# Performance work log

Hardware: AMD Instinct MI355X
Metric: run time of the kernel (lower is better)

Reference implementation:

```python
import jax, jax.numpy as jnp
import numpy as np

N, E, B = 50000, 1600000, 64
VOCAB, EMB = 1000, 16
HID, OUT_FEAT = 192, 128   # hidden_sf*model_dim, out_sf*output_channels
MODEL_DIM, DEMO, OUT_DIM = 64, 5, 2
EPS = 1e-7  # GENConv eps


def setup_inputs() -> dict:
    key = jax.random.key(0)
    ks = jax.random.split(key, 18)
    f32 = jnp.float32

    def rn(k, shape, scale):
        return jax.random.normal(k, shape, dtype=f32) * scale

    node_idx = jax.random.randint(ks[0], (N,), 0, VOCAB)
    edge_index = jax.random.randint(ks[1], (2, E), 0, N)
    batch = jnp.sort(jax.random.randint(ks[2], (N,), 0, B))
    demographics = rn(ks[3], (B, DEMO), 1.0)

    emb = rn(ks[4], (VOCAB, EMB), 1.0)
    dims = [(EMB, HID), (HID, HID), (HID, HID), (HID, OUT_FEAT)]
    params = {}
    for i, (din, dout) in enumerate(dims):
        params[f"W{i}"] = rn(ks[5 + 2 * i], (din, dout), 1.0 / np.sqrt(din))
        params[f"b{i}"] = jnp.zeros((dout,), f32)
    params["Wc1"] = rn(ks[13], (OUT_FEAT + DEMO, MODEL_DIM), 1.0 / np.sqrt(OUT_FEAT + DEMO))
    params["bc1"] = jnp.zeros((MODEL_DIM,), f32)
    params["Wc2"] = rn(ks[14], (MODEL_DIM, OUT_DIM), 1.0 / np.sqrt(MODEL_DIM))
    params["bc2"] = jnp.zeros((OUT_DIM,), f32)

    return {"node_idx": node_idx, "edge_index": edge_index, "batch": batch,
            "demographics": demographics, "emb": emb, **params}


def _gen_conv(x, src, dst, W, b):
    # GENConv (num_layers=1, aggr='add', edge_attr=None):
    #   out_i = Linear( sum_{j->i} (relu(x_j) + eps) + x_i )
    m = jax.nn.relu(x) + EPS                                   # [N, D]
    agg = jax.ops.segment_sum(m[src], dst, num_segments=x.shape[0])
    return (agg + x) @ W + b


def reference(node_idx, edge_index, batch, demographics, emb,
              W0, b0, W1, b1, W2, b2, W3, b3, Wc1, bc1, Wc2, bc2):
    x = emb[node_idx]                                          # [N, 16]
    src, dst = edge_index[0], edge_index[1]
    for W, b in ((W0, b0), (W1, b1), (W2, b2), (W3, b3)):
        x = _gen_conv(x, src, dst, W, b)                       # [N, D_l]
    # global_mean_pool
    cnt = jax.ops.segment_sum(jnp.ones((x.shape[0],), x.dtype), batch, num_segments=B)
    g = jax.ops.segment_sum(x, batch, num_segments=B) / jnp.maximum(cnt, 1.0)[:, None]
    feats = jnp.concatenate([g, demographics], axis=1)         # [B, 133]
    h = jax.nn.relu(feats @ Wc1 + bc1)                         # dropout = identity (eval)
    return h @ Wc2 + bc2                                       # [B, out_dim]
```

## Files before the change

kernel.cpp:

```cpp
#include <hip/hip_runtime.h>
#include <stdint.h>

#define EPS 1e-7f

constexpr int N_NODES = 50000;
constexpr int N_EDGES = 1600000;
constexpr int BATCH = 64;
constexpr int EMB = 16;
constexpr int HID = 192;
constexpr int OUTF = 128;
constexpr int DEMO = 5;
constexpr int MODEL_DIM = 64;
constexpr int OUT_DIM = 2;

constexpr int NPART = 8;
constexpr int PART_NODES = (N_NODES + NPART - 1) / NPART;

constexpr int NBKT = 16;
constexpr int BKT_DIV = (N_NODES + NBKT - 1) / NBKT;
constexpr int NB2 = N_NODES * NBKT;

constexpr int SCAN2_CHUNK = 1024;
constexpr int NCHUNK2 = (NB2 + SCAN2_CHUNK - 1) / SCAN2_CHUNK;

typedef unsigned short bf16_t;
typedef unsigned short u16;
typedef short s8v __attribute__((ext_vector_type(8)));
typedef float f4v __attribute__((ext_vector_type(4)));

static __device__ __forceinline__ float bf2f(bf16_t u) {
  return __uint_as_float(((uint32_t)u) << 16);
}
static __device__ __forceinline__ bf16_t f2bf(float f) {
  uint32_t b = __float_as_uint(f);
  return (bf16_t)((b + 0x7FFFu + ((b >> 16) & 1u)) >> 16);
}

__global__ void emb_gather(const int* __restrict__ idx, const float* __restrict__ emb,
                           bf16_t* __restrict__ x) {
  int t = blockIdx.x * blockDim.x + threadIdx.x;
  if (t >= N_NODES * EMB) return;
  int node = t / EMB, f = t % EMB;
  x[t] = f2bf(emb[idx[node] * EMB + f]);
}

__global__ void hist2_kernel(const int* __restrict__ src, const int* __restrict__ dst,
                             int* __restrict__ hist2) {
  int part = blockIdx.x & (NPART - 1);
  int blk = blockIdx.x >> 3;
  int nthread = (gridDim.x >> 3) * blockDim.x;
  int lo = part * PART_NODES, hi = lo + PART_NODES;
  for (int e = blk * blockDim.x + threadIdx.x; e < N_EDGES; e += nthread) {
    int d = dst[e];
    if (d >= lo && d < hi) atomicAdd(&hist2[d * NBKT + src[e] / BKT_DIV], 1);
  }
}

__global__ void chunk_sum2_kernel(const int* __restrict__ hist2, int* __restrict__ chunk_sum) {
  int t = threadIdx.x;
  int base = blockIdx.x * SCAN2_CHUNK + t * 4;
  int v = 0;
#pragma unroll
  for (int j = 0; j < 4; ++j) {
    int i = base + j;
    if (i < NB2) v += hist2[i];
  }
#pragma unroll
  for (int off = 32; off > 0; off >>= 1) v += __shfl_down(v, off);
  __shared__ int s[4];
  if ((t & 63) == 0) s[t >> 6] = v;
  __syncthreads();
  if (t == 0) chunk_sum[blockIdx.x] = s[0] + s[1] + s[2] + s[3];
}

__global__ void scan_chunks2_kernel(const int* __restrict__ chunk_sum,
                                    int* __restrict__ chunk_off) {
  __shared__ int s[1024];
  int t = threadIdx.x;
  int v = (t < NCHUNK2) ? chunk_sum[t] : 0;
  s[t] = v;
  __syncthreads();
  for (int off = 1; off < 1024; off <<= 1) {
    int u = (t >= off) ? s[t - off] : 0;
    __syncthreads();
    s[t] += u;
    __syncthreads();
  }
  if (t < NCHUNK2) chunk_off[t] = s[t] - v;
}

__global__ void chunk_scan_write2_kernel(const int* __restrict__ hist2,
                                         const int* __restrict__ chunk_off,
                                         int* __restrict__ cursor2,
                                         int* __restrict__ row_start) {
  __shared__ int s[256];
  int t = threadIdx.x;
  int base = blockIdx.x * SCAN2_CHUNK + t * 4;
  int local[4];
  int tsum = 0;
#pragma unroll
  for (int j = 0; j < 4; ++j) {
    int i = base + j;
    local[j] = (i < NB2) ? hist2[i] : 0;
    tsum += local[j];
  }
  s[t] = tsum;
  __syncthreads();
  for (int off = 1; off < 256; off <<= 1) {
    int u = (t >= off) ? s[t - off] : 0;
    __syncthreads();
    s[t] += u;
    __syncthreads();
  }
  int run = chunk_off[blockIdx.x] + s[t] - tsum;
#pragma unroll
  for (int j = 0; j < 4; ++j) {
    int i = base + j;
    if (i < NB2) {
      cursor2[i] = run;
      if ((i & (NBKT - 1)) == 0) row_start[i / NBKT] = run;
      if (i == NB2 - 1) row_start[N_NODES] = run + local[j];
      run += local[j];
    }
  }
}

__global__ void scatter_kernel(const int* __restrict__ src, const int* __restrict__ dst,
                               int* __restrict__ cursor2, u16* __restrict__ csr_src) {
  int part = blockIdx.x & (NPART - 1);
  int blk = blockIdx.x >> 3;
  int nthread = (gridDim.x >> 3) * blockDim.x;
  int lo = part * PART_NODES, hi = lo + PART_NODES;
  for (int e = blk * blockDim.x + threadIdx.x; e < N_EDGES; e += nthread) {
    int d = dst[e];
    if (d >= lo && d < hi) {
      int s = src[e];
      int pos = atomicAdd(&cursor2[d * NBKT + s / BKT_DIV], 1);
      csr_src[pos] = (u16)s;
    }
  }
}

template <int TPN, int NPB>
__global__ void agg2_kernel(const uint32_t* __restrict__ x, const int* __restrict__ row_start,
                            const u16* __restrict__ csr_src, uint32_t* __restrict__ out) {
  int f = threadIdx.x % TPN;
  int node = blockIdx.x * NPB + threadIdx.x / TPN;
  if (node >= N_NODES) return;
  int s0 = row_start[node], s1 = row_start[node + 1];
  float deps = (float)(s1 - s0) * EPS;
  uint32_t xv = x[(size_t)node * TPN + f];
  float a0 = __uint_as_float(xv << 16) + deps;
  float a1 = __uint_as_float(xv & 0xFFFF0000u) + deps;
  int e = s0;
  for (; e + 8 <= s1; e += 8) {
    int idx[8];
#pragma unroll
    for (int j = 0; j < 8; ++j) idx[j] = csr_src[e + j];
    uint32_t v[8];
#pragma unroll
    for (int j = 0; j < 8; ++j) v[j] = x[(size_t)idx[j] * TPN + f];
#pragma unroll
    for (int j = 0; j < 8; ++j) {
      a0 += fmaxf(__uint_as_float(v[j] << 16), 0.f);
      a1 += fmaxf(__uint_as_float(v[j] & 0xFFFF0000u), 0.f);
    }
  }
  for (; e < s1; ++e) {
    uint32_t v = x[(size_t)csr_src[e] * TPN + f];
    a0 += fmaxf(__uint_as_float(v << 16), 0.f);
    a1 += fmaxf(__uint_as_float(v & 0xFFFF0000u), 0.f);
  }
  out[(size_t)node * TPN + f] = (uint32_t)f2bf(a0) | ((uint32_t)f2bf(a1) << 16);
}

__global__ void wprep_kernel(const float* __restrict__ W, int K, int NOUT,
                             bf16_t* __restrict__ Wt) {
  int t = blockIdx.x * blockDim.x + threadIdx.x;
  if (t >= K * NOUT) return;
  int k = t / NOUT, n = t % NOUT;
  Wt[(size_t)n * K + k] = f2bf(W[t]);
}

constexpr int FU_TPN = 24;
constexpr int FU_NPB = 16;
constexpr int FU_LDR = 200;
template <int NOUT, bool OUT_BF16>
__global__ void fused_agg_gemm(const uint4* __restrict__ x, const int* __restrict__ row_start,
                               const u16* __restrict__ csr_src,
                               const bf16_t* __restrict__ Wt, const float* __restrict__ bias,
                               void* __restrict__ outp) {
  constexpr int K = 192;
  constexpr int ROW = 24;
  __shared__ bf16_t tile[FU_NPB * FU_LDR];

  {
    int f = threadIdx.x % FU_TPN;
    int ln = threadIdx.x / FU_TPN;
    int node = blockIdx.x * FU_NPB + ln;
    int s0 = row_start[node], s1 = row_start[node + 1];
    float deps = (float)(s1 - s0) * EPS;
    uint4 xv = x[(size_t)node * ROW + f];
    float a[8];
    {
      uint32_t pk[4] = {xv.x, xv.y, xv.z, xv.w};
#pragma unroll
      for (int q = 0; q < 4; ++q) {
        a[2 * q]     = __uint_as_float(pk[q] << 16) + deps;
        a[2 * q + 1] = __uint_as_float(pk[q] & 0xFFFF0000u) + deps;
      }
    }
    int e = s0;
    for (; e + 4 <= s1; e += 4) {
      int idx[4];
#pragma unroll
      for (int j = 0; j < 4; ++j) idx[j] = csr_src[e + j];
      uint4 v[4];
#pragma unroll
      for (int j = 0; j < 4; ++j) v[j] = x[(size_t)idx[j] * ROW + f];
#pragma unroll
      for (int j = 0; j < 4; ++j) {
        uint32_t pk[4] = {v[j].x, v[j].y, v[j].z, v[j].w};
#pragma unroll
        for (int q = 0; q < 4; ++q) {
          a[2 * q]     += fmaxf(__uint_as_float(pk[q] << 16), 0.f);
          a[2 * q + 1] += fmaxf(__uint_as_float(pk[q] & 0xFFFF0000u), 0.f);
        }
      }
    }
    for (; e < s1; ++e) {
      uint4 v = x[(size_t)csr_src[e] * ROW + f];
      uint32_t pk[4] = {v.x, v.y, v.z, v.w};
#pragma unroll
      for (int q = 0; q < 4; ++q) {
        a[2 * q]     += fmaxf(__uint_as_float(pk[q] << 16), 0.f);
        a[2 * q + 1] += fmaxf(__uint_as_float(pk[q] & 0xFFFF0000u), 0.f);
      }
    }
    uint4 o;
    o.x = (uint32_t)f2bf(a[0]) | ((uint32_t)f2bf(a[1]) << 16);
    o.y = (uint32_t)f2bf(a[2]) | ((uint32_t)f2bf(a[3]) << 16);
    o.z = (uint32_t)f2bf(a[4]) | ((uint32_t)f2bf(a[5]) << 16);
    o.w = (uint32_t)f2bf(a[6]) | ((uint32_t)f2bf(a[7]) << 16);
    *reinterpret_cast<uint4*>(&tile[ln * FU_LDR + f * 8]) = o;
  }
  __syncthreads();

  {
    constexpr int KT = K / 32;
    constexpr int NT = NOUT / 16;
    int wave = threadIdx.x >> 6;
    int lane = threadIdx.x & 63;
    int rlo = lane & 15;
    int kbase = (lane >> 4) * 8;

    s8v af[KT];
#pragma unroll
    for (int kt = 0; kt < KT; ++kt)
      af[kt] = *reinterpret_cast<const s8v*>(&tile[rlo * FU_LDR + kbase + kt * 32]);

    int r0 = (lane >> 4) * 4;
    for (int nt = wave; nt < NT; nt += 6) {
      const bf16_t* wp = Wt + ((size_t)(nt * 16 + rlo)) * K + kbase;
      f4v c = {0.f, 0.f, 0.f, 0.f};
#pragma unroll
      for (int kt = 0; kt < KT; ++kt) {
        s8v b = *(const s8v*)(wp + kt * 32);
        c = __builtin_amdgcn_mfma_f32_16x16x32_bf16(af[kt], b, c, 0, 0, 0);
      }
      int col = nt * 16 + rlo;
      float bv = bias[col];
#pragma unroll
      for (int r = 0; r < 4; ++r) {
        float v = c[r] + bv;
        size_t o = (size_t)(blockIdx.x * FU_NPB + r0 + r) * NOUT + col;
        if constexpr (OUT_BF16) ((bf16_t*)outp)[o] = f2bf(v);
        else                    ((float*)outp)[o] = v;
      }
    }
  }
}

template <int DIN, int DOUT, bool OUT_BF16>
__global__ void gemm_kernel(const bf16_t* __restrict__ in, const float* __restrict__ W,
                            const float* __restrict__ bias, void* __restrict__ outp) {
  constexpr int ROWS = 16;
  __shared__ bf16_t tile[ROWS * DIN];
  int c = threadIdx.x;
  int base = blockIdx.x * ROWS;

  {
    const uint4* gsrc = reinterpret_cast<const uint4*>(in + (size_t)base * DIN);
    uint4* ldst = reinterpret_cast<uint4*>(tile);
    constexpr int NV = ROWS * DIN * 2 / 16;
    for (int i = threadIdx.x; i < NV; i += blockDim.x) ldst[i] = gsrc[i];
  }
  __syncthreads();

  float acc[ROWS];
  float bc = bias[c];
#pragma unroll
  for (int r = 0; r < ROWS; ++r) acc[r] = bc;

  for (int k0 = 0; k0 < DIN; k0 += 8) {
    float w[8];
#pragma unroll
    for (int j = 0; j < 8; ++j) w[j] = W[(size_t)(k0 + j) * DOUT + c];
#pragma unroll
    for (int r = 0; r < ROWS; ++r) {
      uint4 packed = *reinterpret_cast<const uint4*>(&tile[r * DIN + k0]);
      uint32_t pk[4] = {packed.x, packed.y, packed.z, packed.w};
#pragma unroll
      for (int q = 0; q < 4; ++q) {
        float lo = __uint_as_float(pk[q] << 16);
        float hi = __uint_as_float(pk[q] & 0xFFFF0000u);
        acc[r] = fmaf(lo, w[2 * q], acc[r]);
        acc[r] = fmaf(hi, w[2 * q + 1], acc[r]);
      }
    }
  }

#pragma unroll
  for (int r = 0; r < ROWS; ++r) {
    size_t o = (size_t)(base + r) * DOUT + c;
    if constexpr (OUT_BF16) ((bf16_t*)outp)[o] = f2bf(acc[r]);
    else                    ((float*)outp)[o] = acc[r];
  }
}

constexpr int POOL_CHUNK = 100;
__global__ void pool_kernel(const float* __restrict__ x, const int* __restrict__ batch,
                            float* __restrict__ gsum, int* __restrict__ gcnt) {
  int f = threadIdx.x;
  int start = blockIdx.x * POOL_CHUNK;
  if (start >= N_NODES) return;
  int end = min(start + POOL_CHUNK, N_NODES);
  int cur = batch[start];
  float acc = 0.f;
  int cnt = 0;
  for (int i = start; i < end; ++i) {
    int b = batch[i];
    if (b != cur) {
      atomicAdd(&gsum[cur * OUTF + f], acc);
      if (f == 0) atomicAdd(&gcnt[cur], cnt);
      acc = 0.f; cnt = 0; cur = b;
    }
    acc += x[(size_t)i * OUTF + f];
    cnt++;
  }
  atomicAdd(&gsum[cur * OUTF + f], acc);
  if (f == 0) atomicAdd(&gcnt[cur], cnt);
}

__global__ void mlp_kernel(const float* __restrict__ gsum, const int* __restrict__ gcnt,
                           const float* __restrict__ demo,
                           const float* __restrict__ Wc1, const float* __restrict__ bc1,
                           const float* __restrict__ Wc2, const float* __restrict__ bc2,
                           float* __restrict__ out) {
  int b = blockIdx.x;
  int c = threadIdx.x;
  __shared__ float feats[OUTF + DEMO];
  float inv = 1.f / fmaxf((float)gcnt[b], 1.f);
  for (int k = c; k < OUTF; k += MODEL_DIM) feats[k] = gsum[b * OUTF + k] * inv;
  if (c < DEMO) feats[OUTF + c] = demo[b * DEMO + c];
  __syncthreads();
  float s = bc1[c];
#pragma unroll
  for (int k = 0; k < OUTF + DEMO; ++k) s = fmaf(feats[k], Wc1[k * MODEL_DIM + c], s);
  float h = fmaxf(s, 0.f);
  float o0 = h * Wc2[c * OUT_DIM + 0];
  float o1 = h * Wc2[c * OUT_DIM + 1];
#pragma unroll
  for (int off = 32; off > 0; off >>= 1) {
    o0 += __shfl_down(o0, off);
    o1 += __shfl_down(o1, off);
  }
  if (c == 0) {
    out[b * OUT_DIM + 0] = o0 + bc2[0];
    out[b * OUT_DIM + 1] = o1 + bc2[1];
  }
}

extern "C" void kernel_launch(void* const* d_in, const int* in_sizes, int n_in,
                              void* d_out, int out_size, void* d_ws, size_t ws_size,
                              hipStream_t stream) {
  const int*   node_idx = (const int*)d_in[0];
  const int*   edge_index = (const int*)d_in[1];
  const int*   batch = (const int*)d_in[2];
  const float* demo = (const float*)d_in[3];
  const float* emb  = (const float*)d_in[4];
  const float* W0 = (const float*)d_in[5];  const float* b0 = (const float*)d_in[6];
  const float* W1 = (const float*)d_in[7];  const float* b1 = (const float*)d_in[8];
  const float* W2 = (const float*)d_in[9];  const float* b2 = (const float*)d_in[10];
  const float* W3 = (const float*)d_in[11]; const float* b3 = (const float*)d_in[12];
  const float* Wc1 = (const float*)d_in[13]; const float* bc1 = (const float*)d_in[14];
  const float* Wc2 = (const float*)d_in[15]; const float* bc2 = (const float*)d_in[16];
  const int* src = edge_index;
  const int* dst = edge_index + N_EDGES;
  float* out = (float*)d_out;

  char* ws = (char*)d_ws;
  size_t off = 0;
  auto alloc = [&](size_t bytes) {
    void* p = ws + off;
    off += (bytes + 255) & ~size_t(255);
    return p;
  };
  bf16_t* xbf     = (bf16_t*)alloc((size_t)N_NODES * HID * 2);
  bf16_t* xbf2    = (bf16_t*)alloc((size_t)N_NODES * HID * 2);
  bf16_t* xbf0    = (bf16_t*)alloc((size_t)N_NODES * EMB * 2);
  bf16_t* agg0    = (bf16_t*)alloc((size_t)N_NODES * EMB * 2);
  float*  x3      = (float*)alloc((size_t)N_NODES * OUTF * 4);
  u16*   csr_src  = (u16*)alloc((size_t)N_EDGES * 2);
  int*   hist2    = (int*)alloc((size_t)NB2 * 4);
  int*   cursor2  = (int*)alloc((size_t)NB2 * 4);
  int*   row_start= (int*)alloc((size_t)(N_NODES + 1) * 4);
  int*   chunk_sum= (int*)alloc((size_t)NCHUNK2 * 4);
  int*   chunk_off= (int*)alloc((size_t)NCHUNK2 * 4);
  float* gsum     = (float*)alloc((size_t)BATCH * OUTF * 4);
  int*   gcnt     = (int*)alloc((size_t)BATCH * 4);
  bf16_t* Wt1     = (bf16_t*)alloc((size_t)HID * HID * 2);
  bf16_t* Wt2     = (bf16_t*)alloc((size_t)HID * HID * 2);
  bf16_t* Wt3     = (bf16_t*)alloc((size_t)OUTF * HID * 2);

  hipMemsetAsync(hist2, 0, (size_t)NB2 * 4, stream);
  hipMemsetAsync(gsum, 0, (size_t)BATCH * OUTF * 4, stream);
  hipMemsetAsync(gcnt, 0, (size_t)BATCH * 4, stream);

  wprep_kernel<<<(HID * HID + 255) / 256, 256, 0, stream>>>(W1, HID, HID, Wt1);
  wprep_kernel<<<(HID * HID + 255) / 256, 256, 0, stream>>>(W2, HID, HID, Wt2);
  wprep_kernel<<<(HID * OUTF + 255) / 256, 256, 0, stream>>>(W3, HID, OUTF, Wt3);

  hist2_kernel<<<NPART * 256, 256, 0, stream>>>(src, dst, hist2);
  chunk_sum2_kernel<<<NCHUNK2, 256, 0, stream>>>(hist2, chunk_sum);
  scan_chunks2_kernel<<<1, 1024, 0, stream>>>(chunk_sum, chunk_off);
  chunk_scan_write2_kernel<<<NCHUNK2, 256, 0, stream>>>(hist2, chunk_off, cursor2, row_start);
  scatter_kernel<<<NPART * 256, 256, 0, stream>>>(src, dst, cursor2, csr_src);

  constexpr int FU_GRID = N_NODES / FU_NPB;

  emb_gather<<<(N_NODES * EMB + 255) / 256, 256, 0, stream>>>(node_idx, emb, xbf0);
  agg2_kernel<8, 32><<<(N_NODES + 31) / 32, 256, 0, stream>>>(
      (const uint32_t*)xbf0, row_start, csr_src, (uint32_t*)agg0);
  gemm_kernel<16, 192, true><<<N_NODES / 16, 192, 0, stream>>>(agg0, W0, b0, xbf);
  fused_agg_gemm<192, true><<<FU_GRID, FU_TPN * FU_NPB, 0, stream>>>(
      (const uint4*)xbf, row_start, csr_src, Wt1, b1, xbf2);
  fused_agg_gemm<192, true><<<FU_GRID, FU_TPN * FU_NPB, 0, stream>>>(
      (const uint4*)xbf2, row_start, csr_src, Wt2, b2, xbf);
  fused_agg_gemm<128, false><<<FU_GRID, FU_TPN * FU_NPB, 0, stream>>>(
      (const uint4*)xbf, row_start, csr_src, Wt3, b3, x3);

  pool_kernel<<<(N_NODES + POOL_CHUNK - 1) / POOL_CHUNK, OUTF, 0, stream>>>(x3, batch, gsum, gcnt);
  mlp_kernel<<<BATCH, MODEL_DIM, 0, stream>>>(gsum, gcnt, demo, Wc1, bc1, Wc2, bc2, out);
}
```

Baseline: 487.5 us.

## Sort nodes by in-degree so fused agg-GEMM blocks get balanced work

Builds a degree-binned permutation of nodes (histogram, scan, scatter) and has each fused aggregation+GEMM block process nodes of similar degree, writing outputs to the permuted rows. This targets load imbalance and divergence within blocks, where lanes handling high-degree nodes stall others. It adds three small kernels plus an indirection and scattered output rows, which may lose write locality. With random uniform edges the degrees are near-Poisson around 32, so the imbalance being removed is small.

```diff
diff --git a/kernel.cpp b/kernel.cpp
--- a/kernel.cpp
+++ b/kernel.cpp
@@ -22,6 +22,8 @@
 
 constexpr int SCAN2_CHUNK = 1024;
 constexpr int NCHUNK2 = (NB2 + SCAN2_CHUNK - 1) / SCAN2_CHUNK;
+
+constexpr int NDBIN = 1024;
 
 typedef unsigned short bf16_t;
 typedef unsigned short u16;
@@ -138,6 +140,39 @@
       int pos = atomicAdd(&cursor2[d * NBKT + s / BKT_DIV], 1);
       csr_src[pos] = (u16)s;
     }
+  }
+}
+
+__global__ void dbin_hist_kernel(const int* __restrict__ row_start, int* __restrict__ dhist) {
+  int i = blockIdx.x * blockDim.x + threadIdx.x;
+  if (i < N_NODES) {
+    int deg = row_start[i + 1] - row_start[i];
+    atomicAdd(&dhist[min(deg, NDBIN - 1)], 1);
+  }
+}
+
+__global__ void dbin_scan_kernel(const int* __restrict__ dhist, int* __restrict__ dcur) {
+  __shared__ int s[NDBIN];
+  int t = threadIdx.x;
+  int v = dhist[t];
+  s[t] = v;
+  __syncthreads();
+  for (int off = 1; off < NDBIN; off <<= 1) {
+    int u = (t >= off) ? s[t - off] : 0;
+    __syncthreads();
+    s[t] += u;
+    __syncthreads();
+  }
+  dcur[t] = s[t] - v;
+}
+
+__global__ void dbin_scatter_kernel(const int* __restrict__ row_start, int* __restrict__ dcur,
+                                    int* __restrict__ perm) {
+  int i = blockIdx.x * blockDim.x + threadIdx.x;
+  if (i < N_NODES) {
+    int deg = row_start[i + 1] - row_start[i];
+    int pos = atomicAdd(&dcur[min(deg, NDBIN - 1)], 1);
+    perm[pos] = i;
   }
 }
 
@@ -187,17 +222,19 @@
 constexpr int FU_LDR = 200;
 template <int NOUT, bool OUT_BF16>
 __global__ void fused_agg_gemm(const uint4* __restrict__ x, const int* __restrict__ row_start,
-                               const u16* __restrict__ csr_src,
+                               const u16* __restrict__ csr_src, const int* __restrict__ perm,
                                const bf16_t* __restrict__ Wt, const float* __restrict__ bias,
                                void* __restrict__ outp) {
   constexpr int K = 192;
   constexpr int ROW = 24;
   __shared__ bf16_t tile[FU_NPB * FU_LDR];
+  __shared__ int nodemap[FU_NPB];
 
   {
     int f = threadIdx.x % FU_TPN;
     int ln = threadIdx.x / FU_TPN;
-    int node = blockIdx.x * FU_NPB + ln;
+    int node = perm[blockIdx.x * FU_NPB + ln];
+    if (f == 0) nodemap[ln] = node;
     int s0 = row_start[node], s1 = row_start[node + 1];
     float deps = (float)(s1 - s0) * EPS;
     uint4 xv = x[(size_t)node * ROW + f];
@@ -260,6 +297,10 @@
       af[kt] = *reinterpret_cast<const s8v*>(&tile[rlo * FU_LDR + kbase + kt * 32]);
 
     int r0 = (lane >> 4) * 4;
+    int orow[4];
+#pragma unroll
+    for (int r = 0; r < 4; ++r) orow[r] = nodemap[r0 + r];
+
     for (int nt = wave; nt < NT; nt += 6) {
       const bf16_t* wp = Wt + ((size_t)(nt * 16 + rlo)) * K + kbase;
       f4v c = {0.f, 0.f, 0.f, 0.f};
@@ -273,7 +314,7 @@
 #pragma unroll
       for (int r = 0; r < 4; ++r) {
         float v = c[r] + bv;
-        size_t o = (size_t)(blockIdx.x * FU_NPB + r0 + r) * NOUT + col;
+        size_t o = (size_t)orow[r] * NOUT + col;
         if constexpr (OUT_BF16) ((bf16_t*)outp)[o] = f2bf(v);
         else                    ((float*)outp)[o] = v;
       }
@@ -417,6 +458,9 @@
   int*   row_start= (int*)alloc((size_t)(N_NODES + 1) * 4);
   int*   chunk_sum= (int*)alloc((size_t)NCHUNK2 * 4);
   int*   chunk_off= (int*)alloc((size_t)NCHUNK2 * 4);
+  int*   dhist    = (int*)alloc((size_t)NDBIN * 4);
+  int*   dcur     = (int*)alloc((size_t)NDBIN * 4);
+  int*   perm     = (int*)alloc((size_t)N_NODES * 4);
   float* gsum     = (float*)alloc((size_t)BATCH * OUTF * 4);
   int*   gcnt     = (int*)alloc((size_t)BATCH * 4);
   bf16_t* Wt1     = (bf16_t*)alloc((size_t)HID * HID * 2);
@@ -424,6 +468,7 @@
   bf16_t* Wt3     = (bf16_t*)alloc((size_t)OUTF * HID * 2);
 
   hipMemsetAsync(hist2, 0, (size_t)NB2 * 4, stream);
+  hipMemsetAsync(dhist, 0, (size_t)NDBIN * 4, stream);
   hipMemsetAsync(gsum, 0, (size_t)BATCH * OUTF * 4, stream);
   hipMemsetAsync(gcnt, 0, (size_t)BATCH * 4, stream);
 
@@ -437,6 +482,10 @@
   chunk_scan_write2_kernel<<<NCHUNK2, 256, 0, stream>>>(hist2, chunk_off, cursor2, row_start);
   scatter_kernel<<<NPART * 256, 256, 0, stream>>>(src, dst, cursor2, csr_src);
 
+  dbin_hist_kernel<<<(N_NODES + 255) / 256, 256, 0, stream>>>(row_start, dhist);
+  dbin_scan_kernel<<<1, NDBIN, 0, stream>>>(dhist, dcur);
+  dbin_scatter_kernel<<<(N_NODES + 255) / 256, 256, 0, stream>>>(row_start, dcur, perm);
+
   constexpr int FU_GRID = N_NODES / FU_NPB;
 
   emb_gather<<<(N_NODES * EMB + 255) / 256, 256, 0, stream>>>(node_idx, emb, xbf0);
@@ -444,11 +493,11 @@
       (const uint32_t*)xbf0, row_start, csr_src, (uint32_t*)agg0);
   gemm_kernel<16, 192, true><<<N_NODES / 16, 192, 0, stream>>>(agg0, W0, b0, xbf);
   fused_agg_gemm<192, true><<<FU_GRID, FU_TPN * FU_NPB, 0, stream>>>(
-      (const uint4*)xbf, row_start, csr_src, Wt1, b1, xbf2);
+      (const uint4*)xbf, row_start, csr_src, perm, Wt1, b1, xbf2);
   fused_agg_gemm<192, true><<<FU_GRID, FU_TPN * FU_NPB, 0, stream>>>(
-      (const uint4*)xbf2, row_start, csr_src, Wt2, b2, xbf);
+      (const uint4*)xbf2, row_start, csr_src, perm, Wt2, b2, xbf);
   fused_agg_gemm<128, false><<<FU_GRID, FU_TPN * FU_NPB, 0, stream>>>(
-      (const uint4*)xbf, row_start, csr_src, Wt3, b3, x3);
+      (const uint4*)xbf, row_start, csr_src, perm, Wt3, b3, x3);
 
   pool_kernel<<<(N_NODES + POOL_CHUNK - 1) / POOL_CHUNK, OUTF, 0, stream>>>(x3, batch, gsum, gcnt);
   mlp_kernel<<<BATCH, MODEL_DIM, 0, stream>>>(gsum, gcnt, demo, Wc1, bc1, Wc2, bc2, out);
```

After: 678.9 us. 1.39x slower.
